# Kernel tuning notes

Hardware: AMD Instinct MI355X
Metric: run time of the kernel (lower is better)

The kernel has to match this reference:

```python
import jax, jax.numpy as jnp
import numpy as np

N_NODES = 10000


def _add_self_loops(edge_index, n):
    loops = jnp.arange(n, dtype=edge_index.dtype)
    row = jnp.concatenate([edge_index[0], loops])
    col = jnp.concatenate([edge_index[1], loops])
    return row, col


def _gcn_norm(row, col, n):
    # symmetric normalization: deg^-1/2[row] * deg^-1/2[col], deg counted on col
    deg = jax.ops.segment_sum(jnp.ones_like(col, dtype=jnp.float32), col, num_segments=n)
    dis = jnp.where(deg > 0, jax.lax.rsqrt(jnp.maximum(deg, 1.0)), 0.0)
    return dis[row] * dis[col]


def _gcn_conv(x, W, b, row, col, norm, n):
    h = x @ W                      # [N, out]
    m = h[row] * norm[:, None]     # [E+N, out] gathered, normalized messages
    out = jax.ops.segment_sum(m, col, num_segments=n)
    return out + b


def setup_inputs() -> dict:
    key = jax.random.key(0)
    ks = jax.random.split(key, 10)
    N, E, Cin, Cout = N_NODES, 160000, 256, 512
    x = jax.random.normal(ks[0], (N, Cin), dtype=jnp.float32)
    edge_index = jax.random.randint(ks[1], (2, E), 0, N, dtype=jnp.int64)
    s = 1.0 / np.sqrt(Cin)
    s2 = 1.0 / np.sqrt(Cout)
    return {
        "x": x,
        "edge_index": edge_index,
        "W1": jax.random.normal(ks[2], (Cin, Cout), dtype=jnp.float32) * s,
        "b1": jnp.zeros((Cout,), dtype=jnp.float32),
        "W2": jax.random.normal(ks[3], (Cout, Cout), dtype=jnp.float32) * s2,
        "b2": jnp.zeros((Cout,), dtype=jnp.float32),
        "W3": jax.random.normal(ks[4], (Cout, Cout), dtype=jnp.float32) * s2,
        "b3": jnp.zeros((Cout,), dtype=jnp.float32),
        "W4": jax.random.normal(ks[5], (Cout, Cout), dtype=jnp.float32) * s2,
        "b4": jnp.zeros((Cout,), dtype=jnp.float32),
    }


def reference(x, edge_index, W1, b1, W2, b2, W3, b3, W4, b4):
    n = x.shape[0]
    row, col = _add_self_loops(edge_index, n)
    norm = _gcn_norm(row, col, n)
    h = jax.nn.relu(_gcn_conv(x, W1, b1, row, col, norm, n))
    h = jax.nn.relu(_gcn_conv(h, W2, b2, row, col, norm, n))
    h = jax.nn.relu(_gcn_conv(h, W3, b3, row, col, norm, n))
    h = _gcn_conv(h, W4, b4, row, col, norm, n)
    return h.reshape(-1, 5, h.shape[-1])  # [N/5, 5, 512]
```

## Files before the change

kernel.cpp:

```cpp
#include <hip/hip_runtime.h>
#include <hip/hip_bf16.h>

#define N_NODES 10000
#define N_EDGES 160000

typedef __hip_bfloat16 bf16;
typedef unsigned short u16;
typedef float f32x4 __attribute__((ext_vector_type(4)));
typedef short s16x8 __attribute__((ext_vector_type(8)));
typedef unsigned short us8 __attribute__((ext_vector_type(8)));
typedef unsigned short us4 __attribute__((ext_vector_type(4)));

static __device__ __forceinline__ float b2f(u16 u) {
    unsigned v = (unsigned)u << 16;
    return __uint_as_float(v);
}
static __device__ __forceinline__ u16 f2b(float f) {
    bf16 b = __float2bfloat16(f);
    return *reinterpret_cast<u16*>(&b);
}

#define GLDS(gp, lp)                                                         \
    __builtin_amdgcn_global_load_lds(                                        \
        (const __attribute__((address_space(1))) void*)(const void*)(gp),    \
        (__attribute__((address_space(3))) void*)(lp), 16, 0, 0)


__global__ void k_prep(const int* __restrict__ ei, const float* __restrict__ x,
                       u16* __restrict__ xb,
                       int* __restrict__ row, int* __restrict__ col,
                       int* __restrict__ deg) {
    int t = blockIdx.x * 256 + threadIdx.x;
    float4 v = *(const float4*)(x + (size_t)t * 4);
    us4 st;
    st[0] = f2b(v.x); st[1] = f2b(v.y); st[2] = f2b(v.z); st[3] = f2b(v.w);
    *(us4*)(xb + (size_t)t * 4) = st;

    if (t < N_EDGES) {
        bool is64 = true;
#pragma unroll
        for (int k = 0; k < 8; ++k) is64 = is64 && (ei[2 * k + 1] == 0);
        int r, c;
        if (is64) {
            r = ei[2 * t];
            c = ei[2 * (N_EDGES + t)];
        } else {
            r = ei[t];
            c = ei[N_EDGES + t];
        }
        row[t] = r;
        col[t] = c;
        atomicAdd(&deg[c], 1);
    }
}

__global__ void k_scan_all(const int* __restrict__ deg, float* __restrict__ dis,
                           int* __restrict__ off, int* __restrict__ cur) {
    __shared__ int sd[N_NODES];
    __shared__ int sums[256];
    int t = threadIdx.x;
    for (int i = t; i < N_NODES; i += 256) {
        int d = deg[i];
        sd[i] = d;
        dis[i] = rsqrtf((float)d + 1.0f);
    }
    __syncthreads();
    const int seg = (N_NODES + 255) >> 8;
    int lo = t * seg, hi = lo + seg;
    if (lo > N_NODES) lo = N_NODES;
    if (hi > N_NODES) hi = N_NODES;
    int s = 0;
    for (int i = lo; i < hi; ++i) s += sd[i];
    sums[t] = s;
    __syncthreads();
    for (int d = 1; d < 256; d <<= 1) {
        int v = (t >= d) ? sums[t - d] : 0;
        __syncthreads();
        sums[t] += v;
        __syncthreads();
    }
    int run = sums[t] - s;
    for (int i = lo; i < hi; ++i) {
        off[i] = run;
        cur[i] = run;
        run += sd[i];
    }
    if (t == 255) off[N_NODES] = sums[255];
}


__global__ void k_fill_t(const int* __restrict__ row, const int* __restrict__ col,
                         const float* __restrict__ dis, int* cur,
                         int* __restrict__ crow, float* __restrict__ cnorm,
                         const float* __restrict__ W1, const float* __restrict__ W2,
                         const float* __restrict__ W3, const float* __restrict__ W4,
                         u16* __restrict__ T1, u16* __restrict__ T2,
                         u16* __restrict__ T3, u16* __restrict__ T4) {
    __shared__ u16 tile[32][33];
    if (blockIdx.x < 625) {
        int e = blockIdx.x * 256 + threadIdx.x;
        if (e < N_EDGES) {
            int r = row[e], c = col[e];
            int p = atomicAdd(&cur[c], 1);
            crow[p] = r;
            cnorm[p] = dis[r] * dis[c];
        }
        return;
    }
    int b = blockIdx.x - 625;
    int z = b >> 8;
    int rem = b & 255;
    int by = rem >> 4, bx = rem & 15;
    const float* W = (z == 0) ? W1 : (z == 1) ? W2 : (z == 2) ? W3 : W4;
    u16* WT        = (z == 0) ? T1 : (z == 1) ? T2 : (z == 2) ? T3 : T4;
    int K = (z == 0) ? 256 : 512;
    int k0 = by * 32;
    if (k0 >= K) return;
    int n0 = bx * 32;
    int tx = threadIdx.x & 31, ty = threadIdx.x >> 5;
    for (int i = 0; i < 32; i += 8)
        tile[ty + i][tx] = f2b(W[(size_t)(k0 + ty + i) * 512 + n0 + tx]);
    __syncthreads();
    for (int i = 0; i < 32; i += 8)
        WT[(size_t)(n0 + ty + i) * K + k0 + tx] = tile[tx][ty + i];
}


template <int CE> struct VecT;
template <> struct VecT<4> { typedef us4 T; };
template <> struct VecT<8> { typedef us8 T; };

template <int CE>
__global__ void k_agg(const u16* __restrict__ in, u16* __restrict__ out,
                      const int* __restrict__ off, const int* __restrict__ crow,
                      const float* __restrict__ cnorm, const float* __restrict__ dis) {
    typedef typename VecT<CE>::T VT;
    const int C = CE * 64;
    int node = blockIdx.x * 4 + (threadIdx.x >> 6);
    int lane = threadIdx.x & 63;
    int c = lane * CE;

    float d = dis[node];
    VT sv = *(const VT*)(in + (size_t)node * C + c);
    float a0[CE], a1[CE], a2[CE], a3[CE];
#pragma unroll
    for (int j = 0; j < CE; ++j) {
        a0[j] = b2f(sv[j]) * d * d;
        a1[j] = 0.f; a2[j] = 0.f; a3[j] = 0.f;
    }

    int b = off[node], e = off[node + 1];
    int i = b;
    for (; i + 3 < e; i += 4) {
        int r0 = crow[i], r1 = crow[i + 1], r2 = crow[i + 2], r3 = crow[i + 3];
        float n0 = cnorm[i], n1 = cnorm[i + 1], n2 = cnorm[i + 2], n3 = cnorm[i + 3];
        VT v0 = *(const VT*)(in + (size_t)r0 * C + c);
        VT v1 = *(const VT*)(in + (size_t)r1 * C + c);
        VT v2 = *(const VT*)(in + (size_t)r2 * C + c);
        VT v3 = *(const VT*)(in + (size_t)r3 * C + c);
#pragma unroll
        for (int j = 0; j < CE; ++j) {
            a0[j] = fmaf(b2f(v0[j]), n0, a0[j]);
            a1[j] = fmaf(b2f(v1[j]), n1, a1[j]);
            a2[j] = fmaf(b2f(v2[j]), n2, a2[j]);
            a3[j] = fmaf(b2f(v3[j]), n3, a3[j]);
        }
    }
    for (; i < e; ++i) {
        int r0 = crow[i];
        float n0 = cnorm[i];
        VT v0 = *(const VT*)(in + (size_t)r0 * C + c);
#pragma unroll
        for (int j = 0; j < CE; ++j) a0[j] = fmaf(b2f(v0[j]), n0, a0[j]);
    }
    VT st;
#pragma unroll
    for (int j = 0; j < CE; ++j) st[j] = f2b((a0[j] + a1[j]) + (a2[j] + a3[j]));
    *(VT*)(out + (size_t)node * C + c) = st;
}


static __device__ __forceinline__ void st_out(float* out, size_t idx, float v) { out[idx] = v; }
static __device__ __forceinline__ void st_out(u16* out, size_t idx, float v) { out[idx] = f2b(v); }

static __device__ __forceinline__ void gemm_stage(
        u16 (*Asb)[128][32], u16 (*Bsb)[128][32],
        const u16* const aG[4], const u16* const bG[4],
        const int aP[4], const int aR[4],
        const int bP[4], const int bR[4], int kk) {
#pragma unroll
    for (int q = 0; q < 4; ++q) GLDS(aG[q] + kk, &Asb[aP[q]][aR[q]][0]);
#pragma unroll
    for (int q = 0; q < 4; ++q) GLDS(bG[q] + kk, &Bsb[bP[q]][bR[q]][0]);
}

static __device__ __forceinline__ void gemm_compute(
        const u16 (*Asb)[128][32], const u16 (*Bsb)[128][32],
        int wm, int wn, int l15, int kq, f32x4 acc[4][4]) {
#pragma unroll
    for (int p = 0; p < 2; ++p) {
        s16x8 a[4], bb[4];
#pragma unroll
        for (int mi = 0; mi < 4; ++mi)
            a[mi] = *(const s16x8*)&Asb[p][wm * 64 + mi * 16 + l15][kq * 8];
#pragma unroll
        for (int ni = 0; ni < 4; ++ni)
            bb[ni] = *(const s16x8*)&Bsb[p][wn * 64 + ni * 16 + l15][kq * 8];
#pragma unroll
        for (int mi = 0; mi < 4; ++mi)
#pragma unroll
            for (int ni = 0; ni < 4; ++ni)
                acc[mi][ni] = __builtin_amdgcn_mfma_f32_16x16x32_bf16(
                    a[mi], bb[ni], acc[mi][ni], 0, 0, 0);
    }
}

template <typename OT>
__global__ __launch_bounds__(256, 2) void k_gemm(
        const u16* __restrict__ A, const u16* __restrict__ BT,
        const float* __restrict__ bias, OT* __restrict__ out,
        int M, int K, int NO, int relu) {
    __shared__ u16 As[2][2][128][32];
    __shared__ u16 Bs[2][2][128][32];

    int tid = threadIdx.x;
    int w = tid >> 6;
    int lane = tid & 63;
    int wm = w >> 1, wn = w & 1;
    int m0 = blockIdx.x * 128;
    int n0 = blockIdx.y * 128;
    int l15 = lane & 15;
    int kq = lane >> 4;

    int srow = lane >> 2;
    int skc = (lane & 3) * 8;

    const u16* aG[4]; const u16* bG[4];
    int aP[4], aR[4], bP[4], bR[4];
#pragma unroll
    for (int q = 0; q < 4; ++q) {
        int ca = w * 4 + q;
        aP[q] = ca >> 3;
        aR[q] = (ca & 7) * 16;
        int ar = m0 + aR[q] + srow;
        if (ar > M - 1) ar = M - 1;
        aG[q] = A + (size_t)ar * K + aP[q] * 32 + skc;
        int cb = w * 4 + q;
        bP[q] = cb >> 3;
        bR[q] = (cb & 7) * 16;
        int br = n0 + bR[q] + srow;
        bG[q] = BT + (size_t)br * K + bP[q] * 32 + skc;
    }

    f32x4 acc[4][4];
#pragma unroll
    for (int mi = 0; mi < 4; ++mi)
#pragma unroll
        for (int ni = 0; ni < 4; ++ni) acc[mi][ni] = (f32x4){0.f, 0.f, 0.f, 0.f};

    int NT = K >> 6;
    gemm_stage(As[0], Bs[0], aG, bG, aP, aR, bP, bR, 0);
    __syncthreads();
    for (int t = 0; t < NT; t += 2) {
        gemm_stage(As[1], Bs[1], aG, bG, aP, aR, bP, bR, (t + 1) * 64);
        gemm_compute(As[0], Bs[0], wm, wn, l15, kq, acc);
        __syncthreads();
        if (t + 2 < NT)
            gemm_stage(As[0], Bs[0], aG, bG, aP, aR, bP, bR, (t + 2) * 64);
        gemm_compute(As[1], Bs[1], wm, wn, l15, kq, acc);
        __syncthreads();
    }

    int r0o = (lane >> 4) * 4;
    int cm = m0 + wm * 64;
    int cn = n0 + wn * 64;
    float bv[4];
#pragma unroll
    for (int ni = 0; ni < 4; ++ni) bv[ni] = bias[cn + ni * 16 + l15];
#pragma unroll
    for (int mi = 0; mi < 4; ++mi) {
#pragma unroll
        for (int r = 0; r < 4; ++r) {
            int rowa = cm + mi * 16 + r0o + r;
            if (rowa < M) {
#pragma unroll
                for (int ni = 0; ni < 4; ++ni) {
                    float v = acc[mi][ni][r] + bv[ni];
                    if (relu) v = fmaxf(v, 0.f);
                    st_out(out, (size_t)rowa * NO + cn + ni * 16 + l15, v);
                }
            }
        }
    }
}


extern "C" void kernel_launch(void* const* d_in, const int* in_sizes, int n_in,
                              void* d_out, int out_size, void* d_ws, size_t ws_size,
                              hipStream_t stream) {
    const float* x  = (const float*)d_in[0];
    const int*   ei = (const int*)d_in[1];
    const float* W1 = (const float*)d_in[2];
    const float* b1 = (const float*)d_in[3];
    const float* W2 = (const float*)d_in[4];
    const float* b2 = (const float*)d_in[5];
    const float* W3 = (const float*)d_in[6];
    const float* b3 = (const float*)d_in[7];
    const float* W4 = (const float*)d_in[8];
    const float* b4 = (const float*)d_in[9];

    char* ws = (char*)d_ws;
    size_t o = 0;
    auto alloc = [&](size_t bytes) {
        char* p = ws + o;
        o = (o + bytes + 255) & ~(size_t)255;
        return p;
    };
    int*   row   = (int*)alloc(N_EDGES * 4);
    int*   col   = (int*)alloc(N_EDGES * 4);
    int*   deg   = (int*)alloc(N_NODES * 4);
    float* dis   = (float*)alloc(N_NODES * 4);
    int*   off   = (int*)alloc((N_NODES + 1) * 4);
    int*   cur   = (int*)alloc(N_NODES * 4);
    int*   crow  = (int*)alloc(N_EDGES * 4);
    float* cnorm = (float*)alloc(N_EDGES * 4);
    u16*   WT1   = (u16*)alloc((size_t)512 * 256 * 2);
    u16*   WT2   = (u16*)alloc((size_t)512 * 512 * 2);
    u16*   WT3   = (u16*)alloc((size_t)512 * 512 * 2);
    u16*   WT4   = (u16*)alloc((size_t)512 * 512 * 2);
    u16*   xb    = (u16*)alloc((size_t)N_NODES * 256 * 2);
    u16*   s     = (u16*)alloc((size_t)N_NODES * 512 * 2);
    u16*   h     = (u16*)alloc((size_t)N_NODES * 512 * 2);
    float* outb  = (float*)d_out;

    dim3 b256(256);
    const dim3 gG(79, 4);
    const int  gA = (N_NODES + 3) / 4;
    const int  gP = N_NODES * 256 / 4 / 256;

    hipMemsetAsync(deg, 0, N_NODES * 4, stream);
    k_prep<<<gP, b256, 0, stream>>>(ei, x, xb, row, col, deg);
    k_scan_all<<<1, b256, 0, stream>>>(deg, dis, off, cur);
    k_fill_t<<<625 + 1024, b256, 0, stream>>>(row, col, dis, cur, crow, cnorm,
                                              W1, W2, W3, W4, WT1, WT2, WT3, WT4);

    k_agg<4><<<gA, b256, 0, stream>>>(xb, s, off, crow, cnorm, dis);
    k_gemm<u16><<<gG, b256, 0, stream>>>(s, WT1, b1, h, N_NODES, 256, 512, 1);
    k_agg<8><<<gA, b256, 0, stream>>>(h, s, off, crow, cnorm, dis);
    k_gemm<u16><<<gG, b256, 0, stream>>>(s, WT2, b2, h, N_NODES, 512, 512, 1);
    k_agg<8><<<gA, b256, 0, stream>>>(h, s, off, crow, cnorm, dis);
    k_gemm<u16><<<gG, b256, 0, stream>>>(s, WT3, b3, h, N_NODES, 512, 512, 1);
    k_agg<8><<<gA, b256, 0, stream>>>(h, s, off, crow, cnorm, dis);
    k_gemm<float><<<gG, b256, 0, stream>>>(s, WT4, b4, outb, N_NODES, 512, 512, 0);
}
```

Before: 274.4 us.

## Shrink GEMM tile to 64x128, raise occupancy, and unroll aggregation by eight

The GEMM tile drops from 128x128 to 64x128, with loads split across six chunks per warp, and the grid is reordered so the N dimension varies fastest. The launch bound rises to 3 blocks per SM. This gives more blocks (628 instead of 316) to fill the CUs for a small M and lets consecutive blocks share A rows. The aggregation kernel also gets an 8-edge unrolled loop so more gather loads are in flight. The costs are lower MFMA reuse per LDS load and higher register pressure in the aggregation kernel.

```diff
diff --git a/kernel.cpp b/kernel.cpp
--- a/kernel.cpp
+++ b/kernel.cpp
@@ -151,6 +151,27 @@
 
     int b = off[node], e = off[node + 1];
     int i = b;
+    for (; i + 7 < e; i += 8) {
+        int r[8]; float nn[8]; VT v[8];
+#pragma unroll
+        for (int q = 0; q < 8; ++q) { r[q] = crow[i + q]; nn[q] = cnorm[i + q]; }
+#pragma unroll
+        for (int q = 0; q < 8; ++q) v[q] = *(const VT*)(in + (size_t)r[q] * C + c);
+#pragma unroll
+        for (int j = 0; j < CE; ++j) {
+            a0[j] = fmaf(b2f(v[0][j]), nn[0], a0[j]);
+            a1[j] = fmaf(b2f(v[1][j]), nn[1], a1[j]);
+            a2[j] = fmaf(b2f(v[2][j]), nn[2], a2[j]);
+            a3[j] = fmaf(b2f(v[3][j]), nn[3], a3[j]);
+        }
+#pragma unroll
+        for (int j = 0; j < CE; ++j) {
+            a0[j] = fmaf(b2f(v[4][j]), nn[4], a0[j]);
+            a1[j] = fmaf(b2f(v[5][j]), nn[5], a1[j]);
+            a2[j] = fmaf(b2f(v[6][j]), nn[6], a2[j]);
+            a3[j] = fmaf(b2f(v[7][j]), nn[7], a3[j]);
+        }
+    }
     for (; i + 3 < e; i += 4) {
         int r0 = crow[i], r1 = crow[i + 1], r2 = crow[i + 2], r3 = crow[i + 3];
         float n0 = cnorm[i], n1 = cnorm[i + 1], n2 = cnorm[i + 2], n3 = cnorm[i + 3];
@@ -184,30 +205,30 @@
 static __device__ __forceinline__ void st_out(u16* out, size_t idx, float v) { out[idx] = f2b(v); }
 
 static __device__ __forceinline__ void gemm_stage(
-        u16 (*Asb)[128][32], u16 (*Bsb)[128][32],
-        const u16* const aG[4], const u16* const bG[4],
-        const int aP[4], const int aR[4],
-        const int bP[4], const int bR[4], int kk) {
-#pragma unroll
-    for (int q = 0; q < 4; ++q) GLDS(aG[q] + kk, &Asb[aP[q]][aR[q]][0]);
-#pragma unroll
-    for (int q = 0; q < 4; ++q) GLDS(bG[q] + kk, &Bsb[bP[q]][bR[q]][0]);
+        u16 (*Asb)[64][32], u16 (*Bsb)[128][32],
+        const u16* const G[6], const int isA[6],
+        const int P[6], const int R[6], int kk) {
+#pragma unroll
+    for (int q = 0; q < 6; ++q) {
+        if (isA[q]) GLDS(G[q] + kk, &Asb[P[q]][R[q]][0]);
+        else        GLDS(G[q] + kk, &Bsb[P[q]][R[q]][0]);
+    }
 }
 
 static __device__ __forceinline__ void gemm_compute(
-        const u16 (*Asb)[128][32], const u16 (*Bsb)[128][32],
-        int wm, int wn, int l15, int kq, f32x4 acc[4][4]) {
+        const u16 (*Asb)[64][32], const u16 (*Bsb)[128][32],
+        int wm, int wn, int l15, int kq, f32x4 acc[2][4]) {
 #pragma unroll
     for (int p = 0; p < 2; ++p) {
-        s16x8 a[4], bb[4];
-#pragma unroll
-        for (int mi = 0; mi < 4; ++mi)
-            a[mi] = *(const s16x8*)&Asb[p][wm * 64 + mi * 16 + l15][kq * 8];
+        s16x8 a[2], bb[4];
+#pragma unroll
+        for (int mi = 0; mi < 2; ++mi)
+            a[mi] = *(const s16x8*)&Asb[p][wm * 32 + mi * 16 + l15][kq * 8];
 #pragma unroll
         for (int ni = 0; ni < 4; ++ni)
             bb[ni] = *(const s16x8*)&Bsb[p][wn * 64 + ni * 16 + l15][kq * 8];
 #pragma unroll
-        for (int mi = 0; mi < 4; ++mi)
+        for (int mi = 0; mi < 2; ++mi)
 #pragma unroll
             for (int ni = 0; ni < 4; ++ni)
                 acc[mi][ni] = __builtin_amdgcn_mfma_f32_16x16x32_bf16(
@@ -216,69 +237,74 @@
 }
 
 template <typename OT>
-__global__ __launch_bounds__(256, 2) void k_gemm(
+__global__ __launch_bounds__(256, 3) void k_gemm(
         const u16* __restrict__ A, const u16* __restrict__ BT,
         const float* __restrict__ bias, OT* __restrict__ out,
         int M, int K, int NO, int relu) {
-    __shared__ u16 As[2][2][128][32];
+    __shared__ u16 As[2][2][64][32];
     __shared__ u16 Bs[2][2][128][32];
 
     int tid = threadIdx.x;
     int w = tid >> 6;
     int lane = tid & 63;
     int wm = w >> 1, wn = w & 1;
-    int m0 = blockIdx.x * 128;
-    int n0 = blockIdx.y * 128;
+    int n0 = blockIdx.x * 128;
+    int m0 = blockIdx.y * 64;
     int l15 = lane & 15;
     int kq = lane >> 4;
 
     int srow = lane >> 2;
     int skc = (lane & 3) * 8;
 
-    const u16* aG[4]; const u16* bG[4];
-    int aP[4], aR[4], bP[4], bR[4];
-#pragma unroll
-    for (int q = 0; q < 4; ++q) {
-        int ca = w * 4 + q;
-        aP[q] = ca >> 3;
-        aR[q] = (ca & 7) * 16;
-        int ar = m0 + aR[q] + srow;
-        if (ar > M - 1) ar = M - 1;
-        aG[q] = A + (size_t)ar * K + aP[q] * 32 + skc;
-        int cb = w * 4 + q;
-        bP[q] = cb >> 3;
-        bR[q] = (cb & 7) * 16;
-        int br = n0 + bR[q] + srow;
-        bG[q] = BT + (size_t)br * K + bP[q] * 32 + skc;
-    }
-
-    f32x4 acc[4][4];
-#pragma unroll
-    for (int mi = 0; mi < 4; ++mi)
+    const u16* G[6];
+    int isA[6], P[6], R[6];
+#pragma unroll
+    for (int q = 0; q < 6; ++q) {
+        int ch = w * 6 + q;
+        if (ch < 8) {
+            isA[q] = 1;
+            P[q] = ch >> 2;
+            R[q] = (ch & 3) * 16;
+            int ar = m0 + R[q] + srow;
+            if (ar > M - 1) ar = M - 1;
+            G[q] = A + (size_t)ar * K + P[q] * 32 + skc;
+        } else {
+            int cb = ch - 8;
+            isA[q] = 0;
+            P[q] = cb >> 3;
+            R[q] = (cb & 7) * 16;
+            int br = n0 + R[q] + srow;
+            G[q] = BT + (size_t)br * K + P[q] * 32 + skc;
+        }
+    }
+
+    f32x4 acc[2][4];
+#pragma unroll
+    for (int mi = 0; mi < 2; ++mi)
 #pragma unroll
         for (int ni = 0; ni < 4; ++ni) acc[mi][ni] = (f32x4){0.f, 0.f, 0.f, 0.f};
 
     int NT = K >> 6;
-    gemm_stage(As[0], Bs[0], aG, bG, aP, aR, bP, bR, 0);
+    gemm_stage(As[0], Bs[0], G, isA, P, R, 0);
     __syncthreads();
     for (int t = 0; t < NT; t += 2) {
-        gemm_stage(As[1], Bs[1], aG, bG, aP, aR, bP, bR, (t + 1) * 64);
+        gemm_stage(As[1], Bs[1], G, isA, P, R, (t + 1) * 64);
         gemm_compute(As[0], Bs[0], wm, wn, l15, kq, acc);
         __syncthreads();
         if (t + 2 < NT)
-            gemm_stage(As[0], Bs[0], aG, bG, aP, aR, bP, bR, (t + 2) * 64);
+            gemm_stage(As[0], Bs[0], G, isA, P, R, (t + 2) * 64);
         gemm_compute(As[1], Bs[1], wm, wn, l15, kq, acc);
         __syncthreads();
     }
 
     int r0o = (lane >> 4) * 4;
-    int cm = m0 + wm * 64;
+    int cm = m0 + wm * 32;
     int cn = n0 + wn * 64;
     float bv[4];
 #pragma unroll
     for (int ni = 0; ni < 4; ++ni) bv[ni] = bias[cn + ni * 16 + l15];
 #pragma unroll
-    for (int mi = 0; mi < 4; ++mi) {
+    for (int mi = 0; mi < 2; ++mi) {
 #pragma unroll
         for (int r = 0; r < 4; ++r) {
             int rowa = cm + mi * 16 + r0o + r;
@@ -334,7 +360,7 @@
     float* outb  = (float*)d_out;
 
     dim3 b256(256);
-    const dim3 gG(79, 4);
+    const dim3 gG(4, 157);
     const int  gA = (N_NODES + 3) / 4;
     const int  gP = N_NODES * 256 / 4 / 256;
 
```

Result: faster. 261.2 us (-4.8%).

## Fuse aggregation and GEMM into per-layer kernel with LDS-resident aggregated rows

Applied to the files above, without the earlier changes.

Each layer now runs as one kernel. A block aggregates 16 nodes' neighbour features into LDS, using an XOR swizzle and a wider 8-edge unroll. It then multiplies that 16-row tile by the full transposed weight with MFMA, reading B straight from global memory. This removes the intermediate aggregated buffer's write and read and halves the number of launches. The weight transpose also moves into the prep kernel, away from the edge fill. In exchange, every 16-row block re-reads the whole weight matrix from global memory or cache without LDS staging, so GEMM reuse is much lower than the previous 128x128 tiles.

```diff
diff --git a/kernel.cpp b/kernel.cpp
--- a/kernel.cpp
+++ b/kernel.cpp
@@ -20,94 +20,42 @@
     return *reinterpret_cast<u16*>(&b);
 }
 
-#define GLDS(gp, lp)                                                         \
-    __builtin_amdgcn_global_load_lds(                                        \
-        (const __attribute__((address_space(1))) void*)(const void*)(gp),    \
-        (__attribute__((address_space(3))) void*)(lp), 16, 0, 0)
-
 
 __global__ void k_prep(const int* __restrict__ ei, const float* __restrict__ x,
                        u16* __restrict__ xb,
                        int* __restrict__ row, int* __restrict__ col,
-                       int* __restrict__ deg) {
-    int t = blockIdx.x * 256 + threadIdx.x;
-    float4 v = *(const float4*)(x + (size_t)t * 4);
-    us4 st;
-    st[0] = f2b(v.x); st[1] = f2b(v.y); st[2] = f2b(v.z); st[3] = f2b(v.w);
-    *(us4*)(xb + (size_t)t * 4) = st;
-
-    if (t < N_EDGES) {
-        bool is64 = true;
-#pragma unroll
-        for (int k = 0; k < 8; ++k) is64 = is64 && (ei[2 * k + 1] == 0);
-        int r, c;
-        if (is64) {
-            r = ei[2 * t];
-            c = ei[2 * (N_EDGES + t)];
-        } else {
-            r = ei[t];
-            c = ei[N_EDGES + t];
-        }
-        row[t] = r;
-        col[t] = c;
-        atomicAdd(&deg[c], 1);
-    }
-}
-
-__global__ void k_scan_all(const int* __restrict__ deg, float* __restrict__ dis,
-                           int* __restrict__ off, int* __restrict__ cur) {
-    __shared__ int sd[N_NODES];
-    __shared__ int sums[256];
-    int t = threadIdx.x;
-    for (int i = t; i < N_NODES; i += 256) {
-        int d = deg[i];
-        sd[i] = d;
-        dis[i] = rsqrtf((float)d + 1.0f);
-    }
-    __syncthreads();
-    const int seg = (N_NODES + 255) >> 8;
-    int lo = t * seg, hi = lo + seg;
-    if (lo > N_NODES) lo = N_NODES;
-    if (hi > N_NODES) hi = N_NODES;
-    int s = 0;
-    for (int i = lo; i < hi; ++i) s += sd[i];
-    sums[t] = s;
-    __syncthreads();
-    for (int d = 1; d < 256; d <<= 1) {
-        int v = (t >= d) ? sums[t - d] : 0;
-        __syncthreads();
-        sums[t] += v;
-        __syncthreads();
-    }
-    int run = sums[t] - s;
-    for (int i = lo; i < hi; ++i) {
-        off[i] = run;
-        cur[i] = run;
-        run += sd[i];
-    }
-    if (t == 255) off[N_NODES] = sums[255];
-}
-
-
-__global__ void k_fill_t(const int* __restrict__ row, const int* __restrict__ col,
-                         const float* __restrict__ dis, int* cur,
-                         int* __restrict__ crow, float* __restrict__ cnorm,
-                         const float* __restrict__ W1, const float* __restrict__ W2,
-                         const float* __restrict__ W3, const float* __restrict__ W4,
-                         u16* __restrict__ T1, u16* __restrict__ T2,
-                         u16* __restrict__ T3, u16* __restrict__ T4) {
+                       int* __restrict__ deg,
+                       const float* __restrict__ W1, const float* __restrict__ W2,
+                       const float* __restrict__ W3, const float* __restrict__ W4,
+                       u16* __restrict__ T1, u16* __restrict__ T2,
+                       u16* __restrict__ T3, u16* __restrict__ T4) {
     __shared__ u16 tile[32][33];
-    if (blockIdx.x < 625) {
-        int e = blockIdx.x * 256 + threadIdx.x;
-        if (e < N_EDGES) {
-            int r = row[e], c = col[e];
-            int p = atomicAdd(&cur[c], 1);
-            crow[p] = r;
-            cnorm[p] = dis[r] * dis[c];
+    if (blockIdx.x < 2500) {
+        int t = blockIdx.x * 256 + threadIdx.x;
+        float4 v = *(const float4*)(x + (size_t)t * 4);
+        us4 st;
+        st[0] = f2b(v.x); st[1] = f2b(v.y); st[2] = f2b(v.z); st[3] = f2b(v.w);
+        *(us4*)(xb + (size_t)t * 4) = st;
+
+        if (t < N_EDGES) {
+            bool is64 = true;
+#pragma unroll
+            for (int k = 0; k < 8; ++k) is64 = is64 && (ei[2 * k + 1] == 0);
+            int r, c;
+            if (is64) {
+                r = ei[2 * t];
+                c = ei[2 * (N_EDGES + t)];
+            } else {
+                r = ei[t];
+                c = ei[N_EDGES + t];
+            }
+            row[t] = r;
+            col[t] = c;
+            atomicAdd(&deg[c], 1);
         }
         return;
     }
-    int b = blockIdx.x - 625;
+    int b = blockIdx.x - 2500;
     int z = b >> 8;
     int rem = b & 255;
     int by = rem >> 4, bx = rem & 15;
@@ -125,171 +73,177 @@
         WT[(size_t)(n0 + ty + i) * K + k0 + tx] = tile[tx][ty + i];
 }
 
+__global__ void k_scan_all(const int* __restrict__ deg, float* __restrict__ dis,
+                           int* __restrict__ off, int* __restrict__ cur) {
+    __shared__ int sd[N_NODES];
+    __shared__ int sums[256];
+    int t = threadIdx.x;
+    for (int i = t; i < N_NODES; i += 256) {
+        int d = deg[i];
+        sd[i] = d;
+        dis[i] = rsqrtf((float)d + 1.0f);
+    }
+    __syncthreads();
+    const int seg = (N_NODES + 255) >> 8;
+    int lo = t * seg, hi = lo + seg;
+    if (lo > N_NODES) lo = N_NODES;
+    if (hi > N_NODES) hi = N_NODES;
+    int s = 0;
+    for (int i = lo; i < hi; ++i) s += sd[i];
+    sums[t] = s;
+    __syncthreads();
+    for (int d = 1; d < 256; d <<= 1) {
+        int v = (t >= d) ? sums[t - d] : 0;
+        __syncthreads();
+        sums[t] += v;
+        __syncthreads();
+    }
+    int run = sums[t] - s;
+    for (int i = lo; i < hi; ++i) {
+        off[i] = run;
+        cur[i] = run;
+        run += sd[i];
+    }
+    if (t == 255) off[N_NODES] = sums[255];
+}
+
+
+__global__ void k_fill(const int* __restrict__ row, const int* __restrict__ col,
+                       const float* __restrict__ dis, int* cur,
+                       int* __restrict__ crow, float* __restrict__ cnorm) {
+    int e = blockIdx.x * 256 + threadIdx.x;
+    if (e < N_EDGES) {
+        int r = row[e], c = col[e];
+        int p = atomicAdd(&cur[c], 1);
+        crow[p] = r;
+        cnorm[p] = dis[r] * dis[c];
+    }
+}
+
 
 template <int CE> struct VecT;
 template <> struct VecT<4> { typedef us4 T; };
 template <> struct VecT<8> { typedef us8 T; };
 
-template <int CE>
-__global__ void k_agg(const u16* __restrict__ in, u16* __restrict__ out,
-                      const int* __restrict__ off, const int* __restrict__ crow,
-                      const float* __restrict__ cnorm, const float* __restrict__ dis) {
-    typedef typename VecT<CE>::T VT;
-    const int C = CE * 64;
-    int node = blockIdx.x * 4 + (threadIdx.x >> 6);
-    int lane = threadIdx.x & 63;
-    int c = lane * CE;
-
-    float d = dis[node];
-    VT sv = *(const VT*)(in + (size_t)node * C + c);
-    float a0[CE], a1[CE], a2[CE], a3[CE];
-#pragma unroll
-    for (int j = 0; j < CE; ++j) {
-        a0[j] = b2f(sv[j]) * d * d;
-        a1[j] = 0.f; a2[j] = 0.f; a3[j] = 0.f;
-    }
-
-    int b = off[node], e = off[node + 1];
-    int i = b;
-    for (; i + 3 < e; i += 4) {
-        int r0 = crow[i], r1 = crow[i + 1], r2 = crow[i + 2], r3 = crow[i + 3];
-        float n0 = cnorm[i], n1 = cnorm[i + 1], n2 = cnorm[i + 2], n3 = cnorm[i + 3];
-        VT v0 = *(const VT*)(in + (size_t)r0 * C + c);
-        VT v1 = *(const VT*)(in + (size_t)r1 * C + c);
-        VT v2 = *(const VT*)(in + (size_t)r2 * C + c);
-        VT v3 = *(const VT*)(in + (size_t)r3 * C + c);
-#pragma unroll
-        for (int j = 0; j < CE; ++j) {
-            a0[j] = fmaf(b2f(v0[j]), n0, a0[j]);
-            a1[j] = fmaf(b2f(v1[j]), n1, a1[j]);
-            a2[j] = fmaf(b2f(v2[j]), n2, a2[j]);
-            a3[j] = fmaf(b2f(v3[j]), n3, a3[j]);
-        }
-    }
-    for (; i < e; ++i) {
-        int r0 = crow[i];
-        float n0 = cnorm[i];
-        VT v0 = *(const VT*)(in + (size_t)r0 * C + c);
-#pragma unroll
-        for (int j = 0; j < CE; ++j) a0[j] = fmaf(b2f(v0[j]), n0, a0[j]);
-    }
-    VT st;
-#pragma unroll
-    for (int j = 0; j < CE; ++j) st[j] = f2b((a0[j] + a1[j]) + (a2[j] + a3[j]));
-    *(VT*)(out + (size_t)node * C + c) = st;
-}
-
-
 static __device__ __forceinline__ void st_out(float* out, size_t idx, float v) { out[idx] = v; }
 static __device__ __forceinline__ void st_out(u16* out, size_t idx, float v) { out[idx] = f2b(v); }
 
-static __device__ __forceinline__ void gemm_stage(
-        u16 (*Asb)[128][32], u16 (*Bsb)[128][32],
-        const u16* const aG[4], const u16* const bG[4],
-        const int aP[4], const int aR[4],
-        const int bP[4], const int bR[4], int kk) {
-#pragma unroll
-    for (int q = 0; q < 4; ++q) GLDS(aG[q] + kk, &Asb[aP[q]][aR[q]][0]);
-#pragma unroll
-    for (int q = 0; q < 4; ++q) GLDS(bG[q] + kk, &Bsb[bP[q]][bR[q]][0]);
-}
-
-static __device__ __forceinline__ void gemm_compute(
-        const u16 (*Asb)[128][32], const u16 (*Bsb)[128][32],
-        int wm, int wn, int l15, int kq, f32x4 acc[4][4]) {
-#pragma unroll
-    for (int p = 0; p < 2; ++p) {
-        s16x8 a[4], bb[4];
-#pragma unroll
-        for (int mi = 0; mi < 4; ++mi)
-            a[mi] = *(const s16x8*)&Asb[p][wm * 64 + mi * 16 + l15][kq * 8];
-#pragma unroll
-        for (int ni = 0; ni < 4; ++ni)
-            bb[ni] = *(const s16x8*)&Bsb[p][wn * 64 + ni * 16 + l15][kq * 8];
-#pragma unroll
-        for (int mi = 0; mi < 4; ++mi)
-#pragma unroll
-            for (int ni = 0; ni < 4; ++ni)
-                acc[mi][ni] = __builtin_amdgcn_mfma_f32_16x16x32_bf16(
-                    a[mi], bb[ni], acc[mi][ni], 0, 0, 0);
-    }
-}
-
-template <typename OT>
-__global__ __launch_bounds__(256, 2) void k_gemm(
-        const u16* __restrict__ A, const u16* __restrict__ BT,
-        const float* __restrict__ bias, OT* __restrict__ out,
-        int M, int K, int NO, int relu) {
-    __shared__ u16 As[2][2][128][32];
-    __shared__ u16 Bs[2][2][128][32];
+template <int K, typename OT>
+__global__ __launch_bounds__(256, 3) void k_layer(
+        const u16* __restrict__ X, const u16* __restrict__ WT,
+        const float* __restrict__ bias, OT* __restrict__ Y,
+        const int* __restrict__ off, const int* __restrict__ crow,
+        const float* __restrict__ cnorm, const float* __restrict__ dis,
+        int relu) {
+    constexpr int CE = K / 64;
+    typedef typename VecT<CE>::T VT;
+    __shared__ u16 As[16 * K];
 
     int tid = threadIdx.x;
     int w = tid >> 6;
     int lane = tid & 63;
-    int wm = w >> 1, wn = w & 1;
-    int m0 = blockIdx.x * 128;
-    int n0 = blockIdx.y * 128;
+    int m0 = blockIdx.x * 16;
+
+    const u16* inp = X + lane * CE;
+    for (int rr = 0; rr < 4; ++rr) {
+        int rowl = w * 4 + rr;
+        int node = m0 + rowl;
+        float dn = dis[node];
+        VT sv = *(const VT*)(inp + (size_t)node * K);
+        float a0[CE], a1[CE], a2[CE], a3[CE];
+#pragma unroll
+        for (int j = 0; j < CE; ++j) {
+            a0[j] = b2f(sv[j]) * dn * dn;
+            a1[j] = 0.f; a2[j] = 0.f; a3[j] = 0.f;
+        }
+        int lo = off[node], hi = off[node + 1];
+        int i = lo;
+        for (; i + 7 < hi; i += 8) {
+            int r[8]; float nn[8]; VT v[8];
+#pragma unroll
+            for (int q = 0; q < 8; ++q) { r[q] = crow[i + q]; nn[q] = cnorm[i + q]; }
+#pragma unroll
+            for (int q = 0; q < 8; ++q) v[q] = *(const VT*)(inp + (size_t)r[q] * K);
+#pragma unroll
+            for (int j = 0; j < CE; ++j) {
+                a0[j] = fmaf(b2f(v[0][j]), nn[0], a0[j]);
+                a1[j] = fmaf(b2f(v[1][j]), nn[1], a1[j]);
+                a2[j] = fmaf(b2f(v[2][j]), nn[2], a2[j]);
+                a3[j] = fmaf(b2f(v[3][j]), nn[3], a3[j]);
+            }
+#pragma unroll
+            for (int j = 0; j < CE; ++j) {
+                a0[j] = fmaf(b2f(v[4][j]), nn[4], a0[j]);
+                a1[j] = fmaf(b2f(v[5][j]), nn[5], a1[j]);
+                a2[j] = fmaf(b2f(v[6][j]), nn[6], a2[j]);
+                a3[j] = fmaf(b2f(v[7][j]), nn[7], a3[j]);
+            }
+        }
+        for (; i + 3 < hi; i += 4) {
+            int r0 = crow[i], r1 = crow[i + 1], r2 = crow[i + 2], r3 = crow[i + 3];
+            float n0 = cnorm[i], n1 = cnorm[i + 1], n2 = cnorm[i + 2], n3 = cnorm[i + 3];
+            VT v0 = *(const VT*)(inp + (size_t)r0 * K);
+            VT v1 = *(const VT*)(inp + (size_t)r1 * K);
+            VT v2 = *(const VT*)(inp + (size_t)r2 * K);
+            VT v3 = *(const VT*)(inp + (size_t)r3 * K);
+#pragma unroll
+            for (int j = 0; j < CE; ++j) {
+                a0[j] = fmaf(b2f(v0[j]), n0, a0[j]);
+                a1[j] = fmaf(b2f(v1[j]), n1, a1[j]);
+                a2[j] = fmaf(b2f(v2[j]), n2, a2[j]);
+                a3[j] = fmaf(b2f(v3[j]), n3, a3[j]);
+            }
+        }
+        for (; i < hi; ++i) {
+            int r0 = crow[i];
+            float n0 = cnorm[i];
+            VT v0 = *(const VT*)(inp + (size_t)r0 * K);
+#pragma unroll
+            for (int j = 0; j < CE; ++j) a0[j] = fmaf(b2f(v0[j]), n0, a0[j]);
+        }
+        VT st;
+#pragma unroll
+        for (int j = 0; j < CE; ++j) st[j] = f2b((a0[j] + a1[j]) + (a2[j] + a3[j]));
+        unsigned byteoff = (unsigned)(rowl * K + lane * CE) * 2u;
+        byteoff ^= (unsigned)((rowl & 7) << 4);
+        *(VT*)((char*)As + byteoff) = st;
+    }
+    __syncthreads();
+
     int l15 = lane & 15;
     int kq = lane >> 4;
-
-    int srow = lane >> 2;
-    int skc = (lane & 3) * 8;
-
-    const u16* aG[4]; const u16* bG[4];
-    int aP[4], aR[4], bP[4], bR[4];
-#pragma unroll
-    for (int q = 0; q < 4; ++q) {
-        int ca = w * 4 + q;
-        aP[q] = ca >> 3;
-        aR[q] = (ca & 7) * 16;
-        int ar = m0 + aR[q] + srow;
-        if (ar > M - 1) ar = M - 1;
-        aG[q] = A + (size_t)ar * K + aP[q] * 32 + skc;
-        int cb = w * 4 + q;
-        bP[q] = cb >> 3;
-        bR[q] = (cb & 7) * 16;
-        int br = n0 + bR[q] + srow;
-        bG[q] = BT + (size_t)br * K + bP[q] * 32 + skc;
-    }
-
-    f32x4 acc[4][4];
-#pragma unroll
-    for (int mi = 0; mi < 4; ++mi)
-#pragma unroll
-        for (int ni = 0; ni < 4; ++ni) acc[mi][ni] = (f32x4){0.f, 0.f, 0.f, 0.f};
-
-    int NT = K >> 6;
-    gemm_stage(As[0], Bs[0], aG, bG, aP, aR, bP, bR, 0);
-    __syncthreads();
-    for (int t = 0; t < NT; t += 2) {
-        gemm_stage(As[1], Bs[1], aG, bG, aP, aR, bP, bR, (t + 1) * 64);
-        gemm_compute(As[0], Bs[0], wm, wn, l15, kq, acc);
-        __syncthreads();
-        if (t + 2 < NT)
-            gemm_stage(As[0], Bs[0], aG, bG, aP, aR, bP, bR, (t + 2) * 64);
-        gemm_compute(As[1], Bs[1], wm, wn, l15, kq, acc);
-        __syncthreads();
-    }
-
-    int r0o = (lane >> 4) * 4;
-    int cm = m0 + wm * 64;
-    int cn = n0 + wn * 64;
-    float bv[4];
-#pragma unroll
-    for (int ni = 0; ni < 4; ++ni) bv[ni] = bias[cn + ni * 16 + l15];
-#pragma unroll
-    for (int mi = 0; mi < 4; ++mi) {
-#pragma unroll
-        for (int r = 0; r < 4; ++r) {
-            int rowa = cm + mi * 16 + r0o + r;
-            if (rowa < M) {
-#pragma unroll
-                for (int ni = 0; ni < 4; ++ni) {
-                    float v = acc[mi][ni][r] + bv[ni];
-                    if (relu) v = fmaxf(v, 0.f);
-                    st_out(out, (size_t)rowa * NO + cn + ni * 16 + l15, v);
-                }
-            }
+    f32x4 acc[8];
+#pragma unroll
+    for (int ni = 0; ni < 8; ++ni) acc[ni] = (f32x4){0.f, 0.f, 0.f, 0.f};
+
+    const u16* bbase = WT + (size_t)(w * 128 + l15) * K + kq * 8;
+    unsigned abase0 = (unsigned)(l15 * K + kq * 8) * 2u;
+    unsigned swz = (unsigned)((l15 & 7) << 4);
+
+#pragma unroll 4
+    for (int kb = 0; kb < K / 32; ++kb) {
+        s16x8 a = *(const s16x8*)((const char*)As + ((abase0 + (unsigned)kb * 64u) ^ swz));
+        s16x8 bb[8];
+#pragma unroll
+        for (int ni = 0; ni < 8; ++ni)
+            bb[ni] = *(const s16x8*)(bbase + (size_t)ni * 16 * K + kb * 32);
+#pragma unroll
+        for (int ni = 0; ni < 8; ++ni)
+            acc[ni] = __builtin_amdgcn_mfma_f32_16x16x32_bf16(a, bb[ni], acc[ni], 0, 0, 0);
+    }
+
+    int cn = w * 128;
+    float bv[8];
+#pragma unroll
+    for (int ni = 0; ni < 8; ++ni) bv[ni] = bias[cn + ni * 16 + l15];
+#pragma unroll
+    for (int r = 0; r < 4; ++r) {
+        int node = m0 + kq * 4 + r;
+#pragma unroll
+        for (int ni = 0; ni < 8; ++ni) {
+            float v = acc[ni][r] + bv[ni];
+            if (relu) v = fmaxf(v, 0.f);
+            st_out(Y, (size_t)node * 512 + cn + ni * 16 + l15, v);
         }
     }
 }
@@ -329,27 +283,20 @@
     u16*   WT3   = (u16*)alloc((size_t)512 * 512 * 2);
     u16*   WT4   = (u16*)alloc((size_t)512 * 512 * 2);
     u16*   xb    = (u16*)alloc((size_t)N_NODES * 256 * 2);
-    u16*   s     = (u16*)alloc((size_t)N_NODES * 512 * 2);
     u16*   h     = (u16*)alloc((size_t)N_NODES * 512 * 2);
+    u16*   g     = (u16*)alloc((size_t)N_NODES * 512 * 2);
     float* outb  = (float*)d_out;
 
     dim3 b256(256);
-    const dim3 gG(79, 4);
-    const int  gA = (N_NODES + 3) / 4;
-    const int  gP = N_NODES * 256 / 4 / 256;
 
     hipMemsetAsync(deg, 0, N_NODES * 4, stream);
-    k_prep<<<gP, b256, 0, stream>>>(ei, x, xb, row, col, deg);
+    k_prep<<<2500 + 1024, b256, 0, stream>>>(ei, x, xb, row, col, deg,
+                                             W1, W2, W3, W4, WT1, WT2, WT3, WT4);
     k_scan_all<<<1, b256, 0, stream>>>(deg, dis, off, cur);
-    k_fill_t<<<625 + 1024, b256, 0, stream>>>(row, col, dis, cur, crow, cnorm,
-                                              W1, W2, W3, W4, WT1, WT2, WT3, WT4);
-
-    k_agg<4><<<gA, b256, 0, stream>>>(xb, s, off, crow, cnorm, dis);
-    k_gemm<u16><<<gG, b256, 0, stream>>>(s, WT1, b1, h, N_NODES, 256, 512, 1);
-    k_agg<8><<<gA, b256, 0, stream>>>(h, s, off, crow, cnorm, dis);
-    k_gemm<u16><<<gG, b256, 0, stream>>>(s, WT2, b2, h, N_NODES, 512, 512, 1);
-    k_agg<8><<<gA, b256, 0, stream>>>(h, s, off, crow, cnorm, dis);
-    k_gemm<u16><<<gG, b256, 0, stream>>>(s, WT3, b3, h, N_NODES, 512, 512, 1);
-    k_agg<8><<<gA, b256, 0, stream>>>(h, s, off, crow, cnorm, dis);
-    k_gemm<float><<<gG, b256, 0, stream>>>(s, WT4, b4, outb, N_NODES, 512, 512, 0);
-}
+    k_fill<<<625, b256, 0, stream>>>(row, col, dis, cur, crow, cnorm);
+
+    k_layer<256, u16 ><<<625, b256, 0, stream>>>(xb, WT1, b1, h, off, crow, cnorm, dis, 1);
+    k_layer<512, u16 ><<<625, b256, 0, stream>>>(h,  WT2, b2, g, off, crow, cnorm, dis, 1);
+    k_layer<512, u16 ><<<625, b256, 0, stream>>>(g,  WT3, b3, h, off, crow, cnorm, dis, 1);
+    k_layer<512, float><<<625, b256, 0, stream>>>(h, WT4, b4, outb, off, crow, cnorm, dis, 0);
+}
```

New measurement: 361.0 us. 1.32x slower.
